# Performance work log

Hardware: AMD Instinct MI355X
Metric: run time of the kernel (lower is better)

The kernel has to match this reference:

```python
import jax, jax.numpy as jnp
import numpy as np

HIDDEN = 2048
N_HEADS = 32
N_KV_HEADS = 8
HEAD_DIM = 64
ROPE_THETA = 10000.0
B, S = 1, 2048


def _rope_tables(seq_len, dim, theta):
    inv_freq = 1.0 / theta ** (jnp.arange(0, dim, 2, dtype=jnp.float32) / dim)
    angles = jnp.arange(seq_len, dtype=jnp.float32)[:, None] * inv_freq[None, :]
    return jnp.cos(angles), jnp.sin(angles)  # (S, dim//2)


def _apply_rope(x, cos, sin):
    # x: (B, S, H, D); cos/sin: (S, D//2)
    x1 = x[..., 0::2]
    x2 = x[..., 1::2]
    c = cos[None, :, None, :]
    s = sin[None, :, None, :]
    x1r = x1 * c - x2 * s
    x2r = x1 * s + x2 * c
    return jnp.stack([x1r, x2r], axis=-1).reshape(x.shape)


def setup_inputs() -> dict:
    key = jax.random.key(0)
    k1, k2, k3, k4, k5 = jax.random.split(key, 5)
    hidden_states = jax.random.normal(k1, (B, S, HIDDEN), dtype=jnp.float32)
    # causal mask (B, S, S): True where attention is allowed
    attention_mask = jnp.tril(jnp.ones((S, S), dtype=bool))[None, :, :]
    scale = 1.0 / np.sqrt(HIDDEN)
    wq = jax.random.normal(k2, (HIDDEN, N_HEADS * HEAD_DIM), dtype=jnp.float32) * scale
    wk = jax.random.normal(k3, (HIDDEN, N_KV_HEADS * HEAD_DIM), dtype=jnp.float32) * scale
    wv = jax.random.normal(k4, (HIDDEN, N_KV_HEADS * HEAD_DIM), dtype=jnp.float32) * scale
    wo = jax.random.normal(k5, (N_HEADS * HEAD_DIM, HIDDEN), dtype=jnp.float32) * scale
    return {"hidden_states": hidden_states, "attention_mask": attention_mask,
            "wq": wq, "wk": wk, "wv": wv, "wo": wo}


def reference(hidden_states, attention_mask, wq, wk, wv, wo):
    b, s, _ = hidden_states.shape
    groups = N_HEADS // N_KV_HEADS
    q = (hidden_states @ wq).reshape(b, s, N_HEADS, HEAD_DIM)
    k = (hidden_states @ wk).reshape(b, s, N_KV_HEADS, HEAD_DIM)
    v = (hidden_states @ wv).reshape(b, s, N_KV_HEADS, HEAD_DIM)
    cos, sin = _rope_tables(s, HEAD_DIM, ROPE_THETA)
    q = _apply_rope(q, cos, sin)
    k = _apply_rope(k, cos, sin)
    # GQA: repeat KV heads to match query heads
    k = jnp.repeat(k, groups, axis=2)
    v = jnp.repeat(v, groups, axis=2)
    q = q.transpose(0, 2, 1, 3)  # (b, h, s, d)
    k = k.transpose(0, 2, 1, 3)
    v = v.transpose(0, 2, 1, 3)
    scores = jnp.einsum("bhqd,bhkd->bhqk", q, k) / jnp.sqrt(jnp.float32(HEAD_DIM))
    scores = jnp.where(attention_mask[:, None, :, :], scores, -jnp.inf)
    probs = jax.nn.softmax(scores, axis=-1)
    out = jnp.einsum("bhqk,bhkd->bhqd", probs, v)
    out = out.transpose(0, 2, 1, 3).reshape(b, s, N_HEADS * HEAD_DIM)
    return out @ wo
```

## Files before the change

### kernel.cpp

```cpp
#include <hip/hip_runtime.h>

#define SEQ   2048
#define HID   2048
#define NH    32
#define NKV   8
#define HD    64
#define NQKV  3072

typedef __bf16 bf8_t __attribute__((ext_vector_type(8)));
typedef float  f4_t  __attribute__((ext_vector_type(4)));

__device__ __forceinline__ unsigned short bfbits(__bf16 h) {
  union { __bf16 h; unsigned short u; } v; v.h = h; return v.u;
}

#define GLLDS16(lds, g)                                                 \
  __builtin_amdgcn_global_load_lds(                                     \
      (const __attribute__((address_space(1))) void*)(g),               \
      (__attribute__((address_space(3))) void*)(lds), 16, 0, 0)

__device__ __forceinline__ void trans_body(const float* __restrict__ src,
                                           unsigned short* __restrict__ dst,
                                           int N, int bn, int bk, float* T) {
  const int tr = threadIdx.x >> 4;
  const int tc = (threadIdx.x & 15) * 4;
#pragma unroll
  for (int i = 0; i < 4; ++i) {
    int r = tr + i * 16;
    float4 v = *(const float4*)(src + (bk + r) * N + bn + tc);
    T[r * 65 + tc]     = v.x; T[r * 65 + tc + 1] = v.y;
    T[r * 65 + tc + 2] = v.z; T[r * 65 + tc + 3] = v.w;
  }
  __syncthreads();
#pragma unroll
  for (int i = 0; i < 4; ++i) {
    int n = tr + i * 16;
    ushort4 o;
    o.x = bfbits((__bf16)T[(tc + 0) * 65 + n]);
    o.y = bfbits((__bf16)T[(tc + 1) * 65 + n]);
    o.z = bfbits((__bf16)T[(tc + 2) * 65 + n]);
    o.w = bfbits((__bf16)T[(tc + 3) * 65 + n]);
    *(ushort4*)(dst + (bn + n) * 2048 + bk + tc) = o;
  }
}

__global__ __launch_bounds__(256) void k_prep(
    const float* __restrict__ hs, const float* __restrict__ wq,
    const float* __restrict__ wk, const float* __restrict__ wv,
    const float* __restrict__ wo, unsigned short* __restrict__ Hb,
    unsigned short* __restrict__ Btq, unsigned short* __restrict__ Bto) {
  __shared__ float T[64 * 65];
  const int b = blockIdx.x;
  if (b < 4096) {
    int i = (b * 256 + threadIdx.x) * 4;
    float4 v = *(const float4*)(hs + i);
    ushort4 o;
    o.x = bfbits((__bf16)v.x); o.y = bfbits((__bf16)v.y);
    o.z = bfbits((__bf16)v.z); o.w = bfbits((__bf16)v.w);
    *(ushort4*)(Hb + i) = o;
  } else if (b < 5120) {
    int c = b - 4096;
    trans_body(wq, Btq, 2048, (c & 31) * 64, (c >> 5) * 64, T);
  } else if (b < 5376) {
    int c = b - 5120;
    trans_body(wk, Btq + 2048 * 2048, 512, (c & 7) * 64, (c >> 3) * 64, T);
  } else if (b < 5632) {
    int c = b - 5376;
    trans_body(wv, Btq + 2560 * 2048, 512, (c & 7) * 64, (c >> 3) * 64, T);
  } else {
    int c = b - 5632;
    trans_body(wo, Bto, 2048, (c & 31) * 64, (c >> 5) * 64, T);
  }
}

template <bool ROPE>
__global__ __launch_bounds__(512) void k_gemm(
    const unsigned short* __restrict__ A, const unsigned short* __restrict__ Bt,
    unsigned short* __restrict__ Qb, unsigned short* __restrict__ Kb,
    unsigned short* __restrict__ Vt, float* __restrict__ Co) {
  __shared__ unsigned short Ald[2][8192];
  __shared__ unsigned short Bld[2][8192];
  const int tid = threadIdx.x, lane = tid & 63, wave = tid >> 6;
  const int quad = lane >> 4, l16 = lane & 15;
  const int m0 = blockIdx.y * 128, n0 = blockIdx.x * 128;
  const int wm = (wave >> 1) * 32, wn = (wave & 1) * 64;
  const int lr2 = lane >> 2;
  const int lsw = ((lane & 3) ^ ((lane >> 3) & 3)) * 8;
  const int rsw = (quad ^ ((l16 >> 1) & 3)) * 8;
  f4_t acc[2][4] = {};
  const unsigned short* gaw = A + (m0 + wave * 16 + lr2) * HID + lsw;
  const unsigned short* gbw = Bt + (n0 + wave * 16 + lr2) * HID + lsw;

#define GSTAGE(kt, bb)                                     \
  do {                                                     \
    GLLDS16(&Ald[bb][wave * 512],        gaw + (kt));      \
    GLLDS16(&Ald[bb][4096 + wave * 512], gaw + (kt) + 32); \
    GLLDS16(&Bld[bb][wave * 512],        gbw + (kt));      \
    GLLDS16(&Bld[bb][4096 + wave * 512], gbw + (kt) + 32); \
  } while (0)

  GSTAGE(0, 0);
  for (int kt = 0; kt < HID; kt += 64) {
    const int bb = (kt >> 6) & 1;
    __syncthreads();
    if (kt + 64 < HID) GSTAGE(kt + 64, bb ^ 1);
#pragma unroll
    for (int ks = 0; ks < 2; ++ks) {
      bf8_t af[2], bfr[4];
#pragma unroll
      for (int i = 0; i < 2; ++i)
        af[i] = *(const bf8_t*)(&Ald[bb][ks * 4096 + (wm + 16 * i + l16) * 32 + rsw]);
#pragma unroll
      for (int j = 0; j < 4; ++j)
        bfr[j] = *(const bf8_t*)(&Bld[bb][ks * 4096 + (wn + 16 * j + l16) * 32 + rsw]);
#pragma unroll
      for (int i = 0; i < 2; ++i)
#pragma unroll
        for (int j = 0; j < 4; ++j)
          acc[i][j] = __builtin_amdgcn_mfma_f32_16x16x32_bf16(af[i], bfr[j],
                                                              acc[i][j], 0, 0, 0);
    }
  }
#undef GSTAGE

  if constexpr (!ROPE) {
#pragma unroll
    for (int i = 0; i < 2; ++i)
#pragma unroll
      for (int j = 0; j < 4; ++j)
#pragma unroll
        for (int r = 0; r < 4; ++r)
          Co[(m0 + wm + 16 * i + quad * 4 + r) * HID + n0 + wn + 16 * j + l16] =
              acc[i][j][r];
  } else {
    const int odd = l16 & 1;
#pragma unroll
    for (int j = 0; j < 4; ++j) {
      const int ct = n0 + wn + 16 * j;
      const int c  = ct + l16;
      if (ct < 2560) {
        const int cr = (ct < 2048) ? c : (c - 2048);
        unsigned short* dst =
            ((ct < 2048) ? Qb : Kb) + (cr >> 6) * SEQ * HD + (cr & 63);
        const float freq =
            __builtin_amdgcn_exp2f(-0.20762050593045951f * (float)(c & 62));
#pragma unroll
        for (int i = 0; i < 2; ++i)
#pragma unroll
          for (int r = 0; r < 4; ++r) {
            const int srow = m0 + wm + 16 * i + quad * 4 + r;
            float sn, cs;
            __sincosf((float)srow * freq, &sn, &cs);
            float a = acc[i][j][r];
            float b = __shfl_xor(a, 1);
            float res = odd ? fmaf(b, sn, a * cs) : fmaf(a, cs, -(b * sn));
            dst[srow * HD] = bfbits((__bf16)res);
          }
      } else {
        unsigned short* dst = Vt + (c - 2560) * SEQ;
#pragma unroll
        for (int i = 0; i < 2; ++i)
#pragma unroll
          for (int r = 0; r < 4; ++r)
            dst[m0 + wm + 16 * i + quad * 4 + r] = bfbits((__bf16)acc[i][j][r]);
      }
    }
  }
}

__global__ __launch_bounds__(256) void k_attn(
    const unsigned short* __restrict__ Qb, const unsigned short* __restrict__ Kb,
    const unsigned short* __restrict__ Vt, unsigned short* __restrict__ AO) {
  const int b = blockIdx.x;
  const int h  = b & 31;
  const int tg = 31 - (b >> 5);
  const int wave = threadIdx.x >> 6;
  const int lane = threadIdx.x & 63;
  const int quad = lane >> 4, l16 = lane & 15;
  const int qrow0 = tg * 64 + wave * 16;
  const int hkv = h >> 2;

  __shared__ unsigned short Kl[2][4096];
  __shared__ unsigned short Vl[2][4096];

  const unsigned short* Qh = Qb + (h * SEQ + qrow0) * HD;
  const unsigned short* Kh = Kb + hkv * SEQ * HD;
  const unsigned short* Vh = Vt + hkv * HD * SEQ;

  bf8_t qf0 = *(const bf8_t*)(Qh + l16 * HD + quad * 8);
  bf8_t qf1 = *(const bf8_t*)(Qh + l16 * HD + quad * 8 + 32);
  bf8_t ones;
#pragma unroll
  for (int i = 0; i < 8; ++i) ones[i] = (__bf16)1.0f;

  const int lr2 = lane >> 2;
  const int lswV = (((lane & 3) ^ ((lane >> 3) & 3)) * 8);
  const int lswK = (((lane & 3) ^ (((lane >> 3) & 1) | (((lane >> 5) & 1) << 1))) * 8);
  const int rsw = (quad ^ ((l16 >> 1) & 3)) * 8;
  const int krow = (l16 >> 2) * 8 + (l16 & 3);

#define STAGE(cc, buf)                                                      \
  do {                                                                      \
    _Pragma("unroll")                                                       \
    for (int i_ = 0; i_ < 2; ++i_) {                                        \
      int idx = wave * 2 + i_;                                              \
      int p = idx >> 2, sub = (idx & 3) * 16;                               \
      GLLDS16(&Kl[buf][idx * 512],                                          \
              Kh + ((cc) * 64 + sub + lr2) * HD + p * 32 + lswK);           \
      GLLDS16(&Vl[buf][idx * 512],                                          \
              Vh + (sub + lr2) * SEQ + (cc) * 64 + p * 32 + lswV);          \
    }                                                                       \
  } while (0)

  f4_t o[4] = {};
  f4_t ol = {};
  const int nc = tg + 1;
  STAGE(0, 0);
  for (int c = 0; c < nc; ++c) {
    const int buf = c & 1;
    __syncthreads();
    if (c + 1 < nc) STAGE(c + 1, buf ^ 1);
    const unsigned short* KL = Kl[buf];
    const unsigned short* VL = Vl[buf];
    const bool msk = (c == nc - 1);
    const int kb = c * 64;
    f4_t s[4] = {};
    __builtin_amdgcn_s_setprio(1);
#pragma unroll
    for (int g = 0; g < 4; ++g) {
      const int row = krow + 4 * (g & 1) + 32 * (g >> 1);
      bf8_t k0 = *(const bf8_t*)(KL + row * 32 + rsw);
      bf8_t k1 = *(const bf8_t*)(KL + 2048 + row * 32 + rsw);
      s[g] = __builtin_amdgcn_mfma_f32_16x16x32_bf16(k0, qf0, s[g], 0, 0, 0);
      s[g] = __builtin_amdgcn_mfma_f32_16x16x32_bf16(k1, qf1, s[g], 0, 0, 0);
    }
    __builtin_amdgcn_s_setprio(0);
    bf8_t pf0, pf1;
#pragma unroll
    for (int g = 0; g < 4; ++g) {
      const int kbase = kb + quad * 8 + 4 * (g & 1) + 32 * (g >> 1);
#pragma unroll
      for (int r = 0; r < 4; ++r) {
        float arg = fmaf(s[g][r], 0.18033688011112043f, -11.541560327111707f);
        if (msk && (kbase + r > qrow0 + l16)) arg = -1e30f;
        const float p = __builtin_amdgcn_exp2f(arg);
        const int j = 4 * (g & 1) + r;
        if (g < 2) pf0[j] = (__bf16)p; else pf1[j] = (__bf16)p;
      }
    }
    __builtin_amdgcn_s_setprio(1);
#pragma unroll
    for (int sl = 0; sl < 4; ++sl) {
      bf8_t v0 = *(const bf8_t*)(VL + (sl * 16 + l16) * 32 + rsw);
      bf8_t v1 = *(const bf8_t*)(VL + 2048 + (sl * 16 + l16) * 32 + rsw);
      o[sl] = __builtin_amdgcn_mfma_f32_16x16x32_bf16(pf0, v0, o[sl], 0, 0, 0);
      o[sl] = __builtin_amdgcn_mfma_f32_16x16x32_bf16(pf1, v1, o[sl], 0, 0, 0);
    }
    ol = __builtin_amdgcn_mfma_f32_16x16x32_bf16(pf0, ones, ol, 0, 0, 0);
    ol = __builtin_amdgcn_mfma_f32_16x16x32_bf16(pf1, ones, ol, 0, 0, 0);
    __builtin_amdgcn_s_setprio(0);
  }
#undef STAGE
  float inv[4];
#pragma unroll
  for (int r = 0; r < 4; ++r) inv[r] = __builtin_amdgcn_rcpf(ol[r]);
#pragma unroll
  for (int sl = 0; sl < 4; ++sl)
#pragma unroll
    for (int r = 0; r < 4; ++r)
      AO[(qrow0 + quad * 4 + r) * (NH * HD) + h * HD + sl * 16 + l16] =
          bfbits((__bf16)(o[sl][r] * inv[r]));
}

extern "C" void kernel_launch(void* const* d_in, const int* in_sizes, int n_in,
                              void* d_out, int out_size, void* d_ws, size_t ws_size,
                              hipStream_t stream) {
  const float* hs = (const float*)d_in[0];
  const float* wq = (const float*)d_in[2];
  const float* wk = (const float*)d_in[3];
  const float* wv = (const float*)d_in[4];
  const float* wo = (const float*)d_in[5];
  float* out = (float*)d_out;
  char* ws = (char*)d_ws;

  unsigned short* Hb  = (unsigned short*)(ws);
  unsigned short* AO  = (unsigned short*)(ws);
  unsigned short* Qb  = (unsigned short*)(ws + (8u << 20));
  unsigned short* Kb  = (unsigned short*)(ws + (16u << 20));
  unsigned short* Vt  = (unsigned short*)(ws + (18u << 20));
  unsigned short* Btq = (unsigned short*)(ws + (20u << 20));
  unsigned short* Bto = (unsigned short*)(ws + (32u << 20));

  k_prep<<<dim3(6656), dim3(256), 0, stream>>>(hs, wq, wk, wv, wo, Hb, Btq, Bto);
  k_gemm<true><<<dim3(NQKV / 128, SEQ / 128), dim3(512), 0, stream>>>(
      Hb, Btq, Qb, Kb, Vt, nullptr);
  k_attn<<<dim3(NH * (SEQ / 64)), dim3(256), 0, stream>>>(Qb, Kb, Vt, AO);
  k_gemm<false><<<dim3(HID / 128, SEQ / 128), dim3(512), 0, stream>>>(
      AO, Bto, nullptr, nullptr, nullptr, out);
}
```

Before: 209.3 us.

## Restructure GEMM main loop into fine-grained half-tile pipelined phases

The GEMM K-loop now runs in half-tile (32-wide K) phases instead of one full 64-wide tile per iteration. Each phase reads fragments from LDS, issues the next half-tile's global-to-LDS loads, waits only on older loads through an explicit vmcnt count, and brackets its MFMAs with barriers and s_setprio. The aim is to keep more loads in flight, overlap LDS reads and loads with MFMAs, and replace the single full __syncthreads per tile with lighter barriers. In exchange there are two barriers per phase, and correctness depends on hand-counted vmcnt values and a hand-unrolled prologue and epilogue.

Result: no change. 209.3 us (+0.0%).

```diff
diff --git a/kernel.cpp b/kernel.cpp
--- a/kernel.cpp
+++ b/kernel.cpp
@@ -88,40 +88,57 @@
   const int lsw = ((lane & 3) ^ ((lane >> 3) & 3)) * 8;
   const int rsw = (quad ^ ((l16 >> 1) & 3)) * 8;
   f4_t acc[2][4] = {};
-  const unsigned short* gaw = A + (m0 + wave * 16 + lr2) * HID + lsw;
-  const unsigned short* gbw = Bt + (n0 + wave * 16 + lr2) * HID + lsw;
-
-#define GSTAGE(kt, bb)                                     \
-  do {                                                     \
-    GLLDS16(&Ald[bb][wave * 512],        gaw + (kt));      \
-    GLLDS16(&Ald[bb][4096 + wave * 512], gaw + (kt) + 32); \
-    GLLDS16(&Bld[bb][wave * 512],        gbw + (kt));      \
-    GLLDS16(&Bld[bb][4096 + wave * 512], gbw + (kt) + 32); \
+  const unsigned short* ga = A + (m0 + wave * 16 + lr2) * HID + lsw;
+  const unsigned short* gb = Bt + (n0 + wave * 16 + lr2) * HID + lsw;
+
+#define STG(P, KS, OFF)                                           \
+  do {                                                            \
+    GLLDS16(&Ald[P][(KS) * 4096 + wave * 512], ga + (OFF));       \
+    GLLDS16(&Bld[P][(KS) * 4096 + wave * 512], gb + (OFF));       \
   } while (0)
 
-  GSTAGE(0, 0);
-  for (int kt = 0; kt < HID; kt += 64) {
-    const int bb = (kt >> 6) & 1;
-    __syncthreads();
-    if (kt + 64 < HID) GSTAGE(kt + 64, bb ^ 1);
-#pragma unroll
-    for (int ks = 0; ks < 2; ++ks) {
-      bf8_t af[2], bfr[4];
-#pragma unroll
-      for (int i = 0; i < 2; ++i)
-        af[i] = *(const bf8_t*)(&Ald[bb][ks * 4096 + (wm + 16 * i + l16) * 32 + rsw]);
-#pragma unroll
-      for (int j = 0; j < 4; ++j)
-        bfr[j] = *(const bf8_t*)(&Bld[bb][ks * 4096 + (wn + 16 * j + l16) * 32 + rsw]);
-#pragma unroll
-      for (int i = 0; i < 2; ++i)
-#pragma unroll
-        for (int j = 0; j < 4; ++j)
-          acc[i][j] = __builtin_amdgcn_mfma_f32_16x16x32_bf16(af[i], bfr[j],
-                                                              acc[i][j], 0, 0, 0);
-    }
-  }
-#undef GSTAGE
+#define PHASE(P, KS, STAGE_STMT, W)                                      \
+  do {                                                                   \
+    bf8_t af[2], bfr[4];                                                 \
+    const unsigned short* KA = &Ald[P][(KS) * 4096];                     \
+    const unsigned short* KB = &Bld[P][(KS) * 4096];                     \
+    af[0]  = *(const bf8_t*)(KA + (wm + l16) * 32 + rsw);                \
+    af[1]  = *(const bf8_t*)(KA + (wm + 16 + l16) * 32 + rsw);           \
+    bfr[0] = *(const bf8_t*)(KB + (wn + l16) * 32 + rsw);                \
+    bfr[1] = *(const bf8_t*)(KB + (wn + 16 + l16) * 32 + rsw);           \
+    bfr[2] = *(const bf8_t*)(KB + (wn + 32 + l16) * 32 + rsw);           \
+    bfr[3] = *(const bf8_t*)(KB + (wn + 48 + l16) * 32 + rsw);           \
+    STAGE_STMT;                                                          \
+    asm volatile("s_waitcnt vmcnt(" #W ")" ::: "memory");                \
+    __builtin_amdgcn_s_barrier();                                        \
+    __builtin_amdgcn_s_setprio(1);                                       \
+    _Pragma("unroll")                                                    \
+    for (int i_ = 0; i_ < 2; ++i_)                                       \
+      _Pragma("unroll")                                                  \
+      for (int j_ = 0; j_ < 4; ++j_)                                     \
+        acc[i_][j_] = __builtin_amdgcn_mfma_f32_16x16x32_bf16(           \
+            af[i_], bfr[j_], acc[i_][j_], 0, 0, 0);                      \
+    __builtin_amdgcn_s_setprio(0);                                       \
+    __builtin_amdgcn_s_barrier();                                        \
+  } while (0)
+
+  STG(0, 0, 0); STG(0, 1, 32); STG(1, 0, 64);
+  asm volatile("s_waitcnt vmcnt(4)" ::: "memory");
+  __builtin_amdgcn_s_barrier();
+
+  for (int it = 0; it < 15; ++it) {
+    PHASE(0, 0, STG(1, 1, 96),  4);
+    PHASE(0, 1, STG(0, 0, 128), 4);
+    PHASE(1, 0, STG(0, 1, 160), 4);
+    PHASE(1, 1, STG(1, 0, 192), 4);
+    ga += 128; gb += 128;
+  }
+  PHASE(0, 0, STG(1, 1, 96), 4);
+  PHASE(0, 1, (void)0, 2);
+  PHASE(1, 0, (void)0, 0);
+  PHASE(1, 1, (void)0, 0);
+#undef PHASE
+#undef STG
 
   if constexpr (!ROPE) {
 #pragma unroll
```

## Load K/V tiles directly from global memory instead of LDS double-buffering

Applied to the files above, without the earlier changes.

Removes the shared-memory double-buffered staging of K and V tiles (global_load_lds plus __syncthreads) from the attention kernel. Each wave now reads its K and V fragments straight from global memory into registers. This drops the block-wide barriers and the LDS traffic, but each of the four waves re-reads the same K/V tile from global or L2, and loads are no longer prefetched one chunk ahead, so latency is exposed before the MFMAs.

After: 314.8 us. 1.5x slower.

```diff
diff --git a/kernel.cpp b/kernel.cpp
--- a/kernel.cpp
+++ b/kernel.cpp
@@ -180,9 +180,6 @@
   const int qrow0 = tg * 64 + wave * 16;
   const int hkv = h >> 2;
 
-  __shared__ unsigned short Kl[2][4096];
-  __shared__ unsigned short Vl[2][4096];
-
   const unsigned short* Qh = Qb + (h * SEQ + qrow0) * HD;
   const unsigned short* Kh = Kb + hkv * SEQ * HD;
   const unsigned short* Vh = Vt + hkv * HD * SEQ;
@@ -193,46 +190,29 @@
 #pragma unroll
   for (int i = 0; i < 8; ++i) ones[i] = (__bf16)1.0f;
 
-  const int lr2 = lane >> 2;
-  const int lswV = (((lane & 3) ^ ((lane >> 3) & 3)) * 8);
-  const int lswK = (((lane & 3) ^ (((lane >> 3) & 1) | (((lane >> 5) & 1) << 1))) * 8);
-  const int rsw = (quad ^ ((l16 >> 1) & 3)) * 8;
   const int krow = (l16 >> 2) * 8 + (l16 & 3);
-
-#define STAGE(cc, buf)                                                      \
-  do {                                                                      \
-    _Pragma("unroll")                                                       \
-    for (int i_ = 0; i_ < 2; ++i_) {                                        \
-      int idx = wave * 2 + i_;                                              \
-      int p = idx >> 2, sub = (idx & 3) * 16;                               \
-      GLLDS16(&Kl[buf][idx * 512],                                          \
-              Kh + ((cc) * 64 + sub + lr2) * HD + p * 32 + lswK);           \
-      GLLDS16(&Vl[buf][idx * 512],                                          \
-              Vh + (sub + lr2) * SEQ + (cc) * 64 + p * 32 + lswV);          \
-    }                                                                       \
-  } while (0)
 
   f4_t o[4] = {};
   f4_t ol = {};
   const int nc = tg + 1;
-  STAGE(0, 0);
   for (int c = 0; c < nc; ++c) {
-    const int buf = c & 1;
-    __syncthreads();
-    if (c + 1 < nc) STAGE(c + 1, buf ^ 1);
-    const unsigned short* KL = Kl[buf];
-    const unsigned short* VL = Vl[buf];
     const bool msk = (c == nc - 1);
     const int kb = c * 64;
+    const unsigned short* Kc = Kh + kb * HD;
+
+    bf8_t k0[4], k1[4];
+#pragma unroll
+    for (int g = 0; g < 4; ++g) {
+      const int row = krow + 4 * (g & 1) + 32 * (g >> 1);
+      k0[g] = *(const bf8_t*)(Kc + row * HD + quad * 8);
+      k1[g] = *(const bf8_t*)(Kc + row * HD + quad * 8 + 32);
+    }
     f4_t s[4] = {};
     __builtin_amdgcn_s_setprio(1);
 #pragma unroll
     for (int g = 0; g < 4; ++g) {
-      const int row = krow + 4 * (g & 1) + 32 * (g >> 1);
-      bf8_t k0 = *(const bf8_t*)(KL + row * 32 + rsw);
-      bf8_t k1 = *(const bf8_t*)(KL + 2048 + row * 32 + rsw);
-      s[g] = __builtin_amdgcn_mfma_f32_16x16x32_bf16(k0, qf0, s[g], 0, 0, 0);
-      s[g] = __builtin_amdgcn_mfma_f32_16x16x32_bf16(k1, qf1, s[g], 0, 0, 0);
+      s[g] = __builtin_amdgcn_mfma_f32_16x16x32_bf16(k0[g], qf0, s[g], 0, 0, 0);
+      s[g] = __builtin_amdgcn_mfma_f32_16x16x32_bf16(k1[g], qf1, s[g], 0, 0, 0);
     }
     __builtin_amdgcn_s_setprio(0);
     bf8_t pf0, pf1;
@@ -251,8 +231,8 @@
     __builtin_amdgcn_s_setprio(1);
 #pragma unroll
     for (int sl = 0; sl < 4; ++sl) {
-      bf8_t v0 = *(const bf8_t*)(VL + (sl * 16 + l16) * 32 + rsw);
-      bf8_t v1 = *(const bf8_t*)(VL + 2048 + (sl * 16 + l16) * 32 + rsw);
+      bf8_t v0 = *(const bf8_t*)(Vh + (sl * 16 + l16) * SEQ + kb + quad * 8);
+      bf8_t v1 = *(const bf8_t*)(Vh + (sl * 16 + l16) * SEQ + kb + quad * 8 + 32);
       o[sl] = __builtin_amdgcn_mfma_f32_16x16x32_bf16(pf0, v0, o[sl], 0, 0, 0);
       o[sl] = __builtin_amdgcn_mfma_f32_16x16x32_bf16(pf1, v1, o[sl], 0, 0, 0);
     }
@@ -260,7 +240,6 @@
     ol = __builtin_amdgcn_mfma_f32_16x16x32_bf16(pf1, ones, ol, 0, 0, 0);
     __builtin_amdgcn_s_setprio(0);
   }
-#undef STAGE
   float inv[4];
 #pragma unroll
   for (int r = 0; r < 4; ++r) inv[r] = __builtin_amdgcn_rcpf(ol[r]);
```

## Load K fragments directly to registers and remap GEMM blocks across XCDs

Applied to the files above, without the earlier changes.

The attention kernel stops staging K tiles through LDS. Each lane now loads its K fragments straight from global memory into registers, with a one-chunk register prefetch, while V stays double-buffered in LDS. This removes the LDS write and read round trip for K at the cost of more VGPRs and less-coalesced global loads. Separately, the GEMM remaps block IDs so that blocks on the same XCD share column tiles, aiming to improve L2 reuse.

New measurement: 245.6 us. 17.3% more time.

```diff
diff --git a/kernel.cpp b/kernel.cpp
--- a/kernel.cpp
+++ b/kernel.cpp
@@ -82,7 +82,12 @@
   __shared__ unsigned short Bld[2][8192];
   const int tid = threadIdx.x, lane = tid & 63, wave = tid >> 6;
   const int quad = lane >> 4, l16 = lane & 15;
-  const int m0 = blockIdx.y * 128, n0 = blockIdx.x * 128;
+  const int nbx = gridDim.x, nby = gridDim.y;
+  const int id  = blockIdx.y * nbx + blockIdx.x;
+  const int xcd = id & 7, loc = id >> 3;
+  const int colsPerX = nbx >> 3;
+  const int m0 = (loc % nby) * 128;
+  const int n0 = (xcd * colsPerX + loc / nby) * 128;
   const int wm = (wave >> 1) * 32, wn = (wave & 1) * 64;
   const int lr2 = lane >> 2;
   const int lsw = ((lane & 3) ^ ((lane >> 3) & 3)) * 8;
@@ -180,7 +185,6 @@
   const int qrow0 = tg * 64 + wave * 16;
   const int hkv = h >> 2;
 
-  __shared__ unsigned short Kl[2][4096];
   __shared__ unsigned short Vl[2][4096];
 
   const unsigned short* Qh = Qb + (h * SEQ + qrow0) * HD;
@@ -195,32 +199,44 @@
 
   const int lr2 = lane >> 2;
   const int lswV = (((lane & 3) ^ ((lane >> 3) & 3)) * 8);
-  const int lswK = (((lane & 3) ^ (((lane >> 3) & 1) | (((lane >> 5) & 1) << 1))) * 8);
   const int rsw = (quad ^ ((l16 >> 1) & 3)) * 8;
   const int krow = (l16 >> 2) * 8 + (l16 & 3);
 
-#define STAGE(cc, buf)                                                      \
+#define STAGEV(cc, buf)                                                     \
   do {                                                                      \
     _Pragma("unroll")                                                       \
     for (int i_ = 0; i_ < 2; ++i_) {                                        \
       int idx = wave * 2 + i_;                                              \
       int p = idx >> 2, sub = (idx & 3) * 16;                               \
-      GLLDS16(&Kl[buf][idx * 512],                                          \
-              Kh + ((cc) * 64 + sub + lr2) * HD + p * 32 + lswK);           \
       GLLDS16(&Vl[buf][idx * 512],                                          \
               Vh + (sub + lr2) * SEQ + (cc) * 64 + p * 32 + lswV);          \
     }                                                                       \
   } while (0)
 
+#define LOADK(cc, a0, a1)                                                   \
+  do {                                                                      \
+    _Pragma("unroll")                                                       \
+    for (int g_ = 0; g_ < 4; ++g_) {                                        \
+      const int row_ = krow + 4 * (g_ & 1) + 32 * (g_ >> 1);                \
+      const unsigned short* kp_ = Kh + ((cc) * 64 + row_) * HD + quad * 8;  \
+      a0[g_] = *(const bf8_t*)(kp_);                                        \
+      a1[g_] = *(const bf8_t*)(kp_ + 32);                                   \
+    }                                                                       \
+  } while (0)
+
+  bf8_t kc0[4], kc1[4], kn0[4], kn1[4];
   f4_t o[4] = {};
   f4_t ol = {};
   const int nc = tg + 1;
-  STAGE(0, 0);
+  STAGEV(0, 0);
+  LOADK(0, kc0, kc1);
   for (int c = 0; c < nc; ++c) {
     const int buf = c & 1;
     __syncthreads();
-    if (c + 1 < nc) STAGE(c + 1, buf ^ 1);
-    const unsigned short* KL = Kl[buf];
+    if (c + 1 < nc) {
+      STAGEV(c + 1, buf ^ 1);
+      LOADK(c + 1, kn0, kn1);
+    }
     const unsigned short* VL = Vl[buf];
     const bool msk = (c == nc - 1);
     const int kb = c * 64;
@@ -228,11 +244,8 @@
     __builtin_amdgcn_s_setprio(1);
 #pragma unroll
     for (int g = 0; g < 4; ++g) {
-      const int row = krow + 4 * (g & 1) + 32 * (g >> 1);
-      bf8_t k0 = *(const bf8_t*)(KL + row * 32 + rsw);
-      bf8_t k1 = *(const bf8_t*)(KL + 2048 + row * 32 + rsw);
-      s[g] = __builtin_amdgcn_mfma_f32_16x16x32_bf16(k0, qf0, s[g], 0, 0, 0);
-      s[g] = __builtin_amdgcn_mfma_f32_16x16x32_bf16(k1, qf1, s[g], 0, 0, 0);
+      s[g] = __builtin_amdgcn_mfma_f32_16x16x32_bf16(kc0[g], qf0, s[g], 0, 0, 0);
+      s[g] = __builtin_amdgcn_mfma_f32_16x16x32_bf16(kc1[g], qf1, s[g], 0, 0, 0);
     }
     __builtin_amdgcn_s_setprio(0);
     bf8_t pf0, pf1;
@@ -259,8 +272,13 @@
     ol = __builtin_amdgcn_mfma_f32_16x16x32_bf16(pf0, ones, ol, 0, 0, 0);
     ol = __builtin_amdgcn_mfma_f32_16x16x32_bf16(pf1, ones, ol, 0, 0, 0);
     __builtin_amdgcn_s_setprio(0);
-  }
-#undef STAGE
+    if (c + 1 < nc) {
+#pragma unroll
+      for (int g = 0; g < 4; ++g) { kc0[g] = kn0[g]; kc1[g] = kn1[g]; }
+    }
+  }
+#undef STAGEV
+#undef LOADK
   float inv[4];
 #pragma unroll
   for (int r = 0; r < 4; ++r) inv[r] = __builtin_amdgcn_rcpf(ol[r]);
```
